# Kernel tuning notes

Hardware: AMD Instinct MI355X
Metric: run time of the kernel (lower is better)

Reference implementation:

```python
import jax, jax.numpy as jnp
import numpy as np

MIN_STD = 1e-05
LEAKY_SLOPE = 0.01


def setup_inputs() -> dict:
    key = jax.random.key(0)
    ks = jax.random.split(key, 8)
    T, B, F, H, A = 512, 256, 64, 256, 8
    s_in = 1.0 / np.sqrt(F)
    s_h = 1.0 / np.sqrt(H)
    return {
        "x": jax.random.normal(ks[0], (T, B, F), jnp.float32),
        "dones": jax.random.randint(ks[1], (T, B), 0, 2, jnp.int32),
        "W1": jax.random.normal(ks[2], (H, F), jnp.float32) * s_in,
        "b1": jnp.zeros((H,), jnp.float32),
        "W_ih": jax.random.normal(ks[3], (3 * H, H), jnp.float32) * s_h,
        "W_hh": jax.random.normal(ks[4], (3 * H, H), jnp.float32) * s_h,
        "b_ih": jnp.zeros((3 * H,), jnp.float32),
        "b_hh": jnp.zeros((3 * H,), jnp.float32),
        "Wm": jax.random.normal(ks[5], (A, H), jnp.float32) * s_h,
        "bm": jnp.zeros((A,), jnp.float32),
        "Ws": jax.random.normal(ks[6], (A, H), jnp.float32) * s_h,
        "bs": jnp.zeros((A,), jnp.float32),
    }


def reference(x, dones, W1, b1, W_ih, W_hh, b_ih, b_hh, Wm, bm, Ws, bs):
    T, B, _ = x.shape
    H = W1.shape[0]

    # shared_net: Linear + LeakyReLU, applied to the whole [T,B,F] tensor
    sf = jnp.einsum('tbf,hf->tbh', x, W1) + b1
    sf = jnp.where(sf >= 0, sf, LEAKY_SLOPE * sf)

    # per-timestep GRU with done-masked hidden reset (PyTorch gate order r,z,n)
    def step(h, inp):
        f_t, d_t = inp                      # f_t: [B,H], d_t: [B]
        h = jnp.where(d_t[:, None] > 0, 0.0, h)
        gi = f_t @ W_ih.T + b_ih            # [B,3H]
        gh = h @ W_hh.T + b_hh              # [B,3H]
        r = jax.nn.sigmoid(gi[:, :H] + gh[:, :H])
        z = jax.nn.sigmoid(gi[:, H:2 * H] + gh[:, H:2 * H])
        n = jnp.tanh(gi[:, 2 * H:] + r * gh[:, 2 * H:])
        h_new = (1.0 - z) * n + z * h
        return h_new, h_new

    h0 = jnp.zeros((B, H), x.dtype)
    h_final, outs = jax.lax.scan(step, h0, (sf, dones))

    # Faithful to source: heads applied to the LAST step's gru_output [1,B,H]
    last = outs[-1][None]                   # [1,B,H]
    means = jnp.tanh(jnp.einsum('sbh,ah->sba', last, Wm) + bm)
    stds = jax.nn.softplus(jnp.einsum('sbh,ah->sba', last, Ws) + bs)
    stds = jnp.maximum(stds, MIN_STD)
    hidden = h_final[None]                  # [num_layers=1, B, H]
    return means, stds, hidden
```

## Files before the change

kernel.cpp:

```cpp
#include <hip/hip_runtime.h>
#include <math.h>

typedef __attribute__((ext_vector_type(8))) _Float16 f16x8;
typedef __attribute__((ext_vector_type(4))) _Float16 f16x4;
typedef __attribute__((ext_vector_type(4))) float f32x4;

#define TT 512
#define BB 256
#define HH 256
#define AA 8

#define OFF_W1   0u
#define OFF_WIH  32768u
#define OFF_WHH  425984u
#define OFF_H    819200u
#define OFF_GI   1081344u
#define GSTRIDE  393216

__device__ inline float fexp2(float x) { return __builtin_amdgcn_exp2f(x); }
__device__ inline float frcp(float x)  { return __builtin_amdgcn_rcpf(x); }
__device__ inline float fsigm(float x) { return frcp(1.f + fexp2(x * -1.4426950408889634f)); }
__device__ inline float ftanh_(float x){ return 1.f - 2.f * frcp(1.f + fexp2(x * 2.8853900817779268f)); }

__global__ __launch_bounds__(256) void prepack(
    const float* __restrict__ W1, const float* __restrict__ Wih,
    const float* __restrict__ Whh, unsigned char* __restrict__ ws) {
  int gid = blockIdx.x * 256 + threadIdx.x;
  int wave = gid >> 6, l = gid & 63;
  const float* src; int K; int tix; size_t dst;
  if (wave < 32)       { src = W1;  K = 64;  tix = wave;       dst = OFF_W1; }
  else if (wave < 416) { src = Wih; K = 256; tix = wave - 32;  dst = OFF_WIH; }
  else                 { src = Whh; K = 256; tix = wave - 416; dst = OFF_WHH; }
  int ntJ = (K == 64) ? 16 : 48;
  int kt = tix / ntJ, jt = tix % ntJ;
  int j;
  if (K == 64) j = jt * 16 + (l & 15);
  else { int g = jt % 3, blk = jt / 3; j = g * 256 + blk * 16 + (l & 15); }
  int k = kt * 32 + (l >> 4) * 8;
  const float* p = src + (size_t)j * K + k;
  f16x8 frag;
#pragma unroll
  for (int e = 0; e < 8; ++e) frag[e] = (_Float16)p[e];
  *(f16x8*)(ws + dst + ((size_t)tix * 64 + l) * 16) = frag;
}

__global__ __launch_bounds__(256) void gru_gi(
    const float* __restrict__ x, const float* __restrict__ b1,
    const float* __restrict__ b_ih, const float* __restrict__ b_hh,
    const unsigned char* __restrict__ wsro, unsigned char* __restrict__ giout,
    int t0) {
  __shared__ __align__(16) _Float16 sfh[2][16 * 256];
  int tid = threadIdx.x, w = tid >> 6, l = tid & 63;
  int tp = blockIdx.x >> 4, bt = blockIdx.x & 15;
  int row = l & 15, kg = l >> 4;

  const f16x8* pW1 = (const f16x8*)(wsro + OFF_W1);
#pragma unroll
  for (int tt = 0; tt < 2; ++tt) {
    int t = t0 + tp * 2 + tt;
    f32x4 sacc[4] = {{0.f,0.f,0.f,0.f},{0.f,0.f,0.f,0.f},{0.f,0.f,0.f,0.f},{0.f,0.f,0.f,0.f}};
    size_t xbase = ((size_t)t * BB + bt * 16 + row) * 64;
#pragma unroll
    for (int kt = 0; kt < 2; ++kt) {
      float4 p0 = *(const float4*)(x + xbase + kt * 32 + kg * 8);
      float4 p1 = *(const float4*)(x + xbase + kt * 32 + kg * 8 + 4);
      float xv[8] = {p0.x, p0.y, p0.z, p0.w, p1.x, p1.y, p1.z, p1.w};
      f16x8 xh;
#pragma unroll
      for (int e = 0; e < 8; ++e) xh[e] = (_Float16)xv[e];
#pragma unroll
      for (int jj = 0; jj < 4; ++jj) {
        f16x8 bw = pW1[(kt * 16 + w * 4 + jj) * 64 + l];
        sacc[jj] = __builtin_amdgcn_mfma_f32_16x16x32_f16(xh, bw, sacc[jj], 0, 0, 0);
      }
    }
#pragma unroll
    for (int jj = 0; jj < 4; ++jj) {
      int j = (w * 4 + jj) * 16 + row;
      float b1v = b1[j];
#pragma unroll
      for (int rg = 0; rg < 4; ++rg) {
        int rr = kg * 4 + rg;
        float v = sacc[jj][rg] + b1v;
        v = v >= 0.f ? v : 0.01f * v;
        int byt = (j * 2) ^ ((rr & 7) << 4);
        *(_Float16*)((char*)sfh[tt] + rr * 512 + byt) = (_Float16)v;
      }
    }
  }
  __syncthreads();

  f32x4 gacc[2][12];
#pragma unroll
  for (int tt = 0; tt < 2; ++tt)
#pragma unroll
    for (int jj = 0; jj < 12; ++jj) gacc[tt][jj] = (f32x4){0.f, 0.f, 0.f, 0.f};
  const f16x8* pWih = (const f16x8*)(wsro + OFF_WIH);
  for (int kt = 0; kt < 8; ++kt) {
    int rb = row * 512 + ((kt * 64 + kg * 16) ^ ((row & 7) << 4));
    f16x8 ah0 = *(const f16x8*)((const char*)sfh[0] + rb);
    f16x8 ah1 = *(const f16x8*)((const char*)sfh[1] + rb);
#pragma unroll
    for (int jj = 0; jj < 12; ++jj) {
      f16x8 bw = pWih[((size_t)(kt * 48 + w * 12 + jj)) * 64 + l];
      gacc[0][jj] = __builtin_amdgcn_mfma_f32_16x16x32_f16(ah0, bw, gacc[0][jj], 0, 0, 0);
      gacc[1][jj] = __builtin_amdgcn_mfma_f32_16x16x32_f16(ah1, bw, gacc[1][jj], 0, 0, 0);
    }
  }
  float biasv[12];
#pragma unroll
  for (int jj = 0; jj < 12; ++jj) {
    int jt = w * 12 + jj;
    int g = jt % 3, blk = jt / 3;
    int j = g * 256 + blk * 16 + row;
    biasv[jj] = b_ih[j] + (g < 2 ? b_hh[j] : 0.f);
  }
#pragma unroll
  for (int tt = 0; tt < 2; ++tt) {
    unsigned char* gbase =
        giout + (size_t)((tp * 2 + tt) * 16 + bt) * 24576 + (l >> 5) * 12288;
#pragma unroll
    for (int jj = 0; jj < 12; ++jj) {
      int jt = w * 12 + jj;
      f16x4 o;
#pragma unroll
      for (int rg = 0; rg < 4; ++rg) o[rg] = (_Float16)(gacc[tt][jj][rg] + biasv[jj]);
      *(f16x4*)(gbase + jt * 256 + (l & 31) * 8) = o;
    }
  }
}

__global__
__attribute__((amdgpu_flat_work_group_size(512, 512), amdgpu_waves_per_eu(2, 2)))
void gru_seq(
    const int* __restrict__ dones, const float* __restrict__ b_hh,
    const float* __restrict__ Wm, const float* __restrict__ bm,
    const float* __restrict__ Wsv, const float* __restrict__ bsv,
    const unsigned char* __restrict__ wsro, unsigned char* __restrict__ hcar,
    const unsigned char* __restrict__ gi, int t0, int tch,
    float* __restrict__ out) {
  __shared__ __align__(16) unsigned char hbuf[2][8192];
  __shared__ unsigned char dnb[2048];
  int tid = threadIdx.x, w = tid >> 6, u = tid & 63;
  int bt8 = blockIdx.x, bt16 = bt8 >> 1, half = bt8 & 1;
  int row16 = u & 15, kg = u >> 4;
  int col16 = u & 15, rgrp = (u >> 4) & 1, blk = u >> 5;
  int c = (2 * w + blk) * 16 + col16;

  f16x8 whh[6][8];
  const f16x8* pWhh = (const f16x8*)(wsro + OFF_WHH);
#pragma unroll
  for (int jj = 0; jj < 6; ++jj)
#pragma unroll
    for (int kt = 0; kt < 8; ++kt)
      whh[jj][kt] = pWhh[(size_t)(kt * 48 + 6 * w + jj) * 64 + u];

  float bn = b_hh[512 + c];

  int ab0 = (kg * 256 + row16 * 16) ^ (kg << 4);
  int ab1 = ab0 ^ 64;
  int ku2 = c >> 3, e2 = c & 7;
  int wbase = (ku2 * 256 + rgrp * 64 + e2 * 2) ^ ((ku2 & 7) << 4);
  const char* hro = (const char*)hbuf;

  float h_old[4];
#pragma unroll
  for (int rg = 0; rg < 4; ++rg) {
    float hv = ((const float*)hcar)[(bt8 * 8 + rgrp * 4 + rg) * 256 + c];
    h_old[rg] = hv;
    int a0 = wbase ^ (rg << 4);
    *(_Float16*)((char*)hbuf + a0) = (_Float16)hv;
    *(_Float16*)((char*)hbuf + (a0 ^ 128)) = (_Float16)hv;
  }

#pragma unroll
  for (int ii = 0; ii < 4; ++ii) {
    int ix = ii * 512 + tid;
    if (ix < tch * 8) {
      int ti = t0 + (ix >> 3) + 1;
      dnb[ix] = (ti < TT) ? (unsigned char)(dones[ti * BB + bt8 * 8 + (ix & 7)] != 0) : (unsigned char)0;
    }
  }

  const unsigned char* gpt = gi + (size_t)bt16 * 24576 + half * 12288 +
                             (2 * w + blk) * 768 + (u & 31) * 8;
  f16x4 gA[3], gB[3];
#pragma unroll
  for (int g = 0; g < 3; ++g) gA[g] = *(const f16x4*)(gpt + g * 256);

  asm volatile("s_waitcnt lgkmcnt(0)" ::: "memory");
  __builtin_amdgcn_s_barrier();

#define STEP(TL, P, GC, GN)                                                     \
  {                                                                             \
    int tn = (TL) + 1 < tch ? (TL) + 1 : tch - 1;                               \
    const unsigned char* gpn = gpt + (size_t)tn * GSTRIDE;                      \
    GN[0] = *(const f16x4*)(gpn);                                               \
    GN[1] = *(const f16x4*)(gpn + 256);                                         \
    GN[2] = *(const f16x4*)(gpn + 512);                                         \
    f32x4 acc[6];                                                               \
    _Pragma("unroll") for (int jj = 0; jj < 6; ++jj)                            \
        acc[jj] = (f32x4){0.f, 0.f, 0.f, 0.f};                                  \
    _Pragma("unroll") for (int kt = 0; kt < 8; ++kt) {                          \
      f16x8 ah = *(const f16x8*)(hro + (P) * 8192 + kt * 1024 +                 \
                                 ((kt & 1) ? ab1 : ab0));                       \
      _Pragma("unroll") for (int jj = 0; jj < 6; ++jj)                          \
        acc[jj] = __builtin_amdgcn_mfma_f32_16x16x32_f16(ah, whh[jj][kt],       \
                                                         acc[jj], 0, 0, 0);     \
    }                                                                           \
    int dn4 = *(const int*)(dnb + (TL) * 8 + rgrp * 4);                         \
    char* hw = (char*)hbuf + ((P) ^ 1) * 8192;                                  \
    _Pragma("unroll") for (int rg = 0; rg < 4; ++rg) {                          \
      float avr = blk ? acc[3][rg] : acc[0][rg];                                \
      float avz = blk ? acc[4][rg] : acc[1][rg];                                \
      float avn = blk ? acc[5][rg] : acc[2][rg];                                \
      float rs = fsigm((float)GC[0][rg] + avr);                                 \
      float zs = fsigm((float)GC[1][rg] + avz);                                 \
      float ng = ftanh_((float)GC[2][rg] + rs * (avn + bn));                    \
      float hn = ng + zs * (h_old[rg] - ng);                                    \
      hn = ((dn4 >> (rg * 8)) & 0xff) ? 0.f : hn;                               \
      h_old[rg] = hn;                                                           \
      int a0 = wbase ^ (rg << 4);                                               \
      *(_Float16*)(hw + a0) = (_Float16)hn;                                     \
      *(_Float16*)(hw + (a0 ^ 128)) = (_Float16)hn;                             \
    }                                                                           \
    asm volatile("s_waitcnt lgkmcnt(0)" ::: "memory");                          \
    __builtin_amdgcn_s_barrier();                                               \
  }

  for (int tl = 0; tl < tch; tl += 2) {
    STEP(tl, 0, gA, gB);
    STEP(tl + 1, 1, gB, gA);
  }
#undef STEP

#pragma unroll
  for (int rg = 0; rg < 4; ++rg)
    ((float*)hcar)[(bt8 * 8 + rgrp * 4 + rg) * 256 + c] = h_old[rg];

  if (t0 + tch == TT) {
#pragma unroll
    for (int rg = 0; rg < 4; ++rg)
      out[2 * BB * AA + (bt8 * 8 + rgrp * 4 + rg) * 256 + c] = h_old[rg];
    if (tid < 128) {
      int r2 = tid >> 4, a = (tid >> 1) & 7, hd = tid & 1;
      const float* W = hd ? Wsv : Wm;
      float acc2 = 0.f;
      for (int k = 0; k < 256; k += 8) {
        int ku = k >> 3;
        f16x8 vh = *(const f16x8*)(hro + ((ku * 256 + r2 * 16) ^ ((ku & 7) << 4)));
#pragma unroll
        for (int e = 0; e < 8; ++e)
          acc2 += (float)vh[e] * W[a * 256 + k + e];
      }
      int b = bt8 * 8 + r2;
      if (hd == 0) {
        out[b * AA + a] = tanhf(acc2 + bm[a]);
      } else {
        float v = acc2 + bsv[a];
        float sp = fmaxf(v, 0.f) + log1pf(expf(-fabsf(v)));
        out[BB * AA + b * AA + a] = fmaxf(sp, 1e-5f);
      }
    }
  }
}

extern "C" void kernel_launch(void* const* d_in, const int* in_sizes, int n_in,
                              void* d_out, int out_size, void* d_ws, size_t ws_size,
                              hipStream_t stream) {
  const float* x    = (const float*)d_in[0];
  const int*   dn   = (const int*)  d_in[1];
  const float* W1   = (const float*)d_in[2];
  const float* b1   = (const float*)d_in[3];
  const float* W_ih = (const float*)d_in[4];
  const float* W_hh = (const float*)d_in[5];
  const float* b_ih = (const float*)d_in[6];
  const float* b_hh = (const float*)d_in[7];
  const float* Wm   = (const float*)d_in[8];
  const float* bm   = (const float*)d_in[9];
  const float* Wsv  = (const float*)d_in[10];
  const float* bs   = (const float*)d_in[11];
  float* out = (float*)d_out;
  unsigned char* ws = (unsigned char*)d_ws;

  int tch = 256;
  while (tch > 1 && (size_t)OFF_GI + (size_t)tch * 16 * 24576 > ws_size) tch >>= 1;

  prepack<<<200, 256, 0, stream>>>(W1, W_ih, W_hh, ws);
  (void)hipMemsetAsync(ws + OFF_H, 0, 262144, stream);
  for (int t0 = 0; t0 < TT; t0 += tch) {
    gru_gi<<<dim3((tch / 2) * 16), 256, 0, stream>>>(x, b1, b_ih, b_hh, ws, ws + OFF_GI, t0);
    gru_seq<<<32, 512, 0, stream>>>(dn, b_hh, Wm, bm, Wsv, bs, ws, ws + OFF_H,
                                    ws + OFF_GI, t0, tch, out);
  }
}
```

Measured before the change: 822.2 us.

## Split GRU recurrence over 64 blocks of 4 batch rows each

```diff
diff --git a/kernel.cpp b/kernel.cpp
--- a/kernel.cpp
+++ b/kernel.cpp
@@ -3,6 +3,7 @@
 
 typedef __attribute__((ext_vector_type(8))) _Float16 f16x8;
 typedef __attribute__((ext_vector_type(4))) _Float16 f16x4;
+typedef __attribute__((ext_vector_type(2))) __fp16 h16x2;
 typedef __attribute__((ext_vector_type(4))) float f32x4;
 
 #define TT 512
@@ -140,11 +141,11 @@
     const unsigned char* __restrict__ gi, int t0, int tch,
     float* __restrict__ out) {
   __shared__ __align__(16) unsigned char hbuf[2][8192];
-  __shared__ unsigned char dnb[2048];
+  __shared__ unsigned char dnb[1024];
   int tid = threadIdx.x, w = tid >> 6, u = tid & 63;
-  int bt8 = blockIdx.x, bt16 = bt8 >> 1, half = bt8 & 1;
+  int bt4 = blockIdx.x, bt16 = bt4 >> 2, q = bt4 & 3;
   int row16 = u & 15, kg = u >> 4;
-  int col16 = u & 15, rgrp = (u >> 4) & 1, blk = u >> 5;
+  int col16 = u & 15, copy = (u >> 4) & 1, blk = u >> 5;
   int c = (2 * w + blk) * 16 + col16;
 
   f16x8 whh[6][8];
@@ -154,39 +155,46 @@
 #pragma unroll
     for (int kt = 0; kt < 8; ++kt)
       whh[jj][kt] = pWhh[(size_t)(kt * 48 + 6 * w + jj) * 64 + u];
+#pragma unroll
+  for (int jj = 0; jj < 6; ++jj)
+#pragma unroll
+    for (int kt = 0; kt < 8; ++kt)
+      asm volatile("" : "+v"(whh[jj][kt]));
 
   float bn = b_hh[512 + c];
 
   int ab0 = (kg * 256 + row16 * 16) ^ (kg << 4);
   int ab1 = ab0 ^ 64;
   int ku2 = c >> 3, e2 = c & 7;
-  int wbase = (ku2 * 256 + rgrp * 64 + e2 * 2) ^ ((ku2 & 7) << 4);
+  int wb = ku2 * 256 + e2 * 2;
+  int sw = (ku2 & 7) << 4;
+  int rb0 = copy * 32;
   const char* hro = (const char*)hbuf;
 
-  float h_old[4];
-#pragma unroll
-  for (int rg = 0; rg < 4; ++rg) {
-    float hv = ((const float*)hcar)[(bt8 * 8 + rgrp * 4 + rg) * 256 + c];
-    h_old[rg] = hv;
-    int a0 = wbase ^ (rg << 4);
-    *(_Float16*)((char*)hbuf + a0) = (_Float16)hv;
-    *(_Float16*)((char*)hbuf + (a0 ^ 128)) = (_Float16)hv;
-  }
-
-#pragma unroll
-  for (int ii = 0; ii < 4; ++ii) {
+  float h_old[2];
+#pragma unroll
+  for (int e = 0; e < 2; ++e) {
+    float hv = ((const float*)hcar)[(bt4 * 4 + 2 * copy + e) * 256 + c];
+    h_old[e] = hv;
+#pragma unroll
+    for (int d = 0; d < 4; ++d)
+      *(_Float16*)((char*)hbuf + ((wb + rb0 + e * 16 + d * 64) ^ sw)) = (_Float16)hv;
+  }
+
+#pragma unroll
+  for (int ii = 0; ii < 2; ++ii) {
     int ix = ii * 512 + tid;
-    if (ix < tch * 8) {
-      int ti = t0 + (ix >> 3) + 1;
-      dnb[ix] = (ti < TT) ? (unsigned char)(dones[ti * BB + bt8 * 8 + (ix & 7)] != 0) : (unsigned char)0;
-    }
-  }
-
-  const unsigned char* gpt = gi + (size_t)bt16 * 24576 + half * 12288 +
-                             (2 * w + blk) * 768 + (u & 31) * 8;
-  f16x4 gA[3], gB[3];
-#pragma unroll
-  for (int g = 0; g < 3; ++g) gA[g] = *(const f16x4*)(gpt + g * 256);
+    if (ix < tch * 4) {
+      int ti = t0 + (ix >> 2) + 1;
+      dnb[ix] = (ti < TT) ? (unsigned char)(dones[ti * BB + bt4 * 4 + (ix & 3)] != 0) : (unsigned char)0;
+    }
+  }
+
+  const unsigned char* gpt = gi + (size_t)bt16 * 24576 + (q >> 1) * 12288 +
+                             (2 * w + blk) * 768 + ((q & 1) * 16 + col16) * 8 + copy * 4;
+  unsigned int gA[3], gB[3];
+#pragma unroll
+  for (int g = 0; g < 3; ++g) gA[g] = *(const unsigned int*)(gpt + g * 256);
 
   asm volatile("s_waitcnt lgkmcnt(0)" ::: "memory");
   __builtin_amdgcn_s_barrier();
@@ -195,9 +203,9 @@
   {                                                                             \
     int tn = (TL) + 1 < tch ? (TL) + 1 : tch - 1;                               \
     const unsigned char* gpn = gpt + (size_t)tn * GSTRIDE;                      \
-    GN[0] = *(const f16x4*)(gpn);                                               \
-    GN[1] = *(const f16x4*)(gpn + 256);                                         \
-    GN[2] = *(const f16x4*)(gpn + 512);                                         \
+    GN[0] = *(const unsigned int*)(gpn);                                        \
+    GN[1] = *(const unsigned int*)(gpn + 256);                                  \
+    GN[2] = *(const unsigned int*)(gpn + 512);                                  \
     f32x4 acc[6];                                                               \
     _Pragma("unroll") for (int jj = 0; jj < 6; ++jj)                            \
         acc[jj] = (f32x4){0.f, 0.f, 0.f, 0.f};                                  \
@@ -208,21 +216,24 @@
         acc[jj] = __builtin_amdgcn_mfma_f32_16x16x32_f16(ah, whh[jj][kt],       \
                                                          acc[jj], 0, 0, 0);     \
     }                                                                           \
-    int dn4 = *(const int*)(dnb + (TL) * 8 + rgrp * 4);                         \
+    int dn2 = *(const unsigned short*)(dnb + (TL) * 4 + copy * 2);              \
     char* hw = (char*)hbuf + ((P) ^ 1) * 8192;                                  \
-    _Pragma("unroll") for (int rg = 0; rg < 4; ++rg) {                          \
-      float avr = blk ? acc[3][rg] : acc[0][rg];                                \
-      float avz = blk ? acc[4][rg] : acc[1][rg];                                \
-      float avn = blk ? acc[5][rg] : acc[2][rg];                                \
-      float rs = fsigm((float)GC[0][rg] + avr);                                 \
-      float zs = fsigm((float)GC[1][rg] + avz);                                 \
-      float ng = ftanh_((float)GC[2][rg] + rs * (avn + bn));                    \
-      float hn = ng + zs * (h_old[rg] - ng);                                    \
-      hn = ((dn4 >> (rg * 8)) & 0xff) ? 0.f : hn;                               \
-      h_old[rg] = hn;                                                           \
-      int a0 = wbase ^ (rg << 4);                                               \
-      *(_Float16*)(hw + a0) = (_Float16)hn;                                     \
-      *(_Float16*)(hw + (a0 ^ 128)) = (_Float16)hn;                             \
+    _Pragma("unroll") for (int e = 0; e < 2; ++e) {                             \
+      float avr = copy ? acc[blk * 3 + 0][2 + e] : acc[blk * 3 + 0][e];         \
+      float avz = copy ? acc[blk * 3 + 1][2 + e] : acc[blk * 3 + 1][e];         \
+      float avn = copy ? acc[blk * 3 + 2][2 + e] : acc[blk * 3 + 2][e];         \
+      float gr = (float)__builtin_bit_cast(h16x2, GC[0])[e];                    \
+      float gz = (float)__builtin_bit_cast(h16x2, GC[1])[e];                    \
+      float gn = (float)__builtin_bit_cast(h16x2, GC[2])[e];                    \
+      float rs = fsigm(gr + avr);                                               \
+      float zs = fsigm(gz + avz);                                               \
+      float ng = ftanh_(gn + rs * (avn + bn));                                  \
+      float hn = ng + zs * (h_old[e] - ng);                                     \
+      hn = ((dn2 >> (e * 8)) & 0xff) ? 0.f : hn;                                \
+      h_old[e] = hn;                                                            \
+      _Float16 hh = (_Float16)hn;                                               \
+      _Pragma("unroll") for (int d = 0; d < 4; ++d)                             \
+        *(_Float16*)(hw + ((wb + rb0 + e * 16 + d * 64) ^ sw)) = hh;            \
     }                                                                           \
     asm volatile("s_waitcnt lgkmcnt(0)" ::: "memory");                          \
     __builtin_amdgcn_s_barrier();                                               \
@@ -235,14 +246,14 @@
 #undef STEP
 
 #pragma unroll
-  for (int rg = 0; rg < 4; ++rg)
-    ((float*)hcar)[(bt8 * 8 + rgrp * 4 + rg) * 256 + c] = h_old[rg];
+  for (int e = 0; e < 2; ++e)
+    ((float*)hcar)[(bt4 * 4 + 2 * copy + e) * 256 + c] = h_old[e];
 
   if (t0 + tch == TT) {
 #pragma unroll
-    for (int rg = 0; rg < 4; ++rg)
-      out[2 * BB * AA + (bt8 * 8 + rgrp * 4 + rg) * 256 + c] = h_old[rg];
-    if (tid < 128) {
+    for (int e = 0; e < 2; ++e)
+      out[2 * BB * AA + (bt4 * 4 + 2 * copy + e) * 256 + c] = h_old[e];
+    if (tid < 64) {
       int r2 = tid >> 4, a = (tid >> 1) & 7, hd = tid & 1;
       const float* W = hd ? Wsv : Wm;
       float acc2 = 0.f;
@@ -253,7 +264,7 @@
         for (int e = 0; e < 8; ++e)
           acc2 += (float)vh[e] * W[a * 256 + k + e];
       }
-      int b = bt8 * 8 + r2;
+      int b = bt4 * 4 + r2;
       if (hd == 0) {
         out[b * AA + a] = tanhf(acc2 + bm[a]);
       } else {
@@ -290,7 +301,7 @@
   (void)hipMemsetAsync(ws + OFF_H, 0, 262144, stream);
   for (int t0 = 0; t0 < TT; t0 += tch) {
     gru_gi<<<dim3((tch / 2) * 16), 256, 0, stream>>>(x, b1, b_ih, b_hh, ws, ws + OFF_GI, t0);
-    gru_seq<<<32, 512, 0, stream>>>(dn, b_hh, Wm, bm, Wsv, bs, ws, ws + OFF_H,
+    gru_seq<<<64, 512, 0, stream>>>(dn, b_hh, Wm, bm, Wsv, bs, ws, ws + OFF_H,
                                     ws + OFF_GI, t0, tch, out);
   }
 }
```

After: 2.463 ms. +199.6%, slower.
